# Performance work log

Measured on AMD Instinct MI355X. Metric: run time of the kernel, lower is better.

## Reference

```python
import jax, jax.numpy as jnp
import numpy as np

D_MODEL, D_INNER, D_STATE, D_CONV, DT_RANK = 192, 384, 16, 4, 12
EPS = 1e-5


def _causal_dwconv(x, w, b):
    # x: (B, L, Din); w: (Din, 1, K) depthwise; causal left pad K-1
    xc = x.transpose(0, 2, 1)  # (B, Din, L)
    y = jax.lax.conv_general_dilated(xc, w, window_strides=(1,),
                                     padding=[(D_CONV - 1, 0)],
                                     feature_group_count=D_INNER,
                                     dimension_numbers=('NCH', 'OIH', 'NCH'))
    return (y + b[None, :, None]).transpose(0, 2, 1)  # (B, L, Din)


def _ssm_dir(xh, z, conv_w, conv_b, x_proj_w, dt_w, dt_b, A_log, D):
    # one direction of the selective scan
    x = jax.nn.silu(_causal_dwconv(xh, conv_w, conv_b))  # (B, L, Din)
    x_dbl = jnp.einsum('bld,ed->ble', x, x_proj_w)       # (B, L, R+2N)
    dt = jax.nn.softplus(jnp.einsum('blr,dr->bld', x_dbl[..., :DT_RANK], dt_w) + dt_b)
    Bm = x_dbl[..., DT_RANK:DT_RANK + D_STATE]           # (B, L, N)
    Cm = x_dbl[..., DT_RANK + D_STATE:]                  # (B, L, N)
    A = -jnp.exp(A_log)                                  # (Din, N)
    deltaA = jnp.exp(dt[..., None] * A)                  # (B, L, Din, N)
    dBx = (dt * x)[..., None] * Bm[:, :, None, :]        # (B, L, Din, N)

    def comb(e1, e2):
        a1, b1 = e1
        a2, b2 = e2
        return a1 * a2, a2 * b1 + b2

    _, h = jax.lax.associative_scan(comb, (deltaA, dBx), axis=1)
    y = jnp.einsum('bldn,bln->bld', h, Cm) + x * D
    return y * jax.nn.silu(z)


def setup_inputs() -> dict:
    key = jax.random.key(0)
    ks = jax.random.split(key, 24)
    B, L = 2, 2048
    s = 0.02
    inp = {
        'hidden_states': jax.random.normal(ks[0], (B, L, D_MODEL), jnp.float32),
        'residual': jax.random.normal(ks[1], (B, L, D_MODEL), jnp.float32),
        'norm_w': jnp.ones((D_MODEL,), jnp.float32),
        'in_proj_w': jax.random.normal(ks[2], (2 * D_INNER, D_MODEL)) * s,
        'out_proj_w': jax.random.normal(ks[3], (D_MODEL, D_INNER)) * s,
        # forward-direction SSM params
        'conv_w_f': jax.random.normal(ks[4], (D_INNER, 1, D_CONV)) * s,
        'conv_b_f': jnp.zeros((D_INNER,), jnp.float32),
        'x_proj_w_f': jax.random.normal(ks[5], (DT_RANK + 2 * D_STATE, D_INNER)) * s,
        'dt_w_f': jax.random.normal(ks[6], (D_INNER, DT_RANK)) * s,
        'dt_b_f': jax.random.uniform(ks[7], (D_INNER,), minval=-4.0, maxval=-2.0),
        'A_log_f': jnp.log(jnp.tile(jnp.arange(1, D_STATE + 1, dtype=jnp.float32), (D_INNER, 1))),
        'D_f': jnp.ones((D_INNER,), jnp.float32),
        # backward-direction SSM params (bimamba)
        'conv_w_b': jax.random.normal(ks[8], (D_INNER, 1, D_CONV)) * s,
        'conv_b_b': jnp.zeros((D_INNER,), jnp.float32),
        'x_proj_w_b': jax.random.normal(ks[9], (DT_RANK + 2 * D_STATE, D_INNER)) * s,
        'dt_w_b': jax.random.normal(ks[10], (D_INNER, DT_RANK)) * s,
        'dt_b_b': jax.random.uniform(ks[11], (D_INNER,), minval=-4.0, maxval=-2.0),
        'A_log_b': jnp.log(jnp.tile(jnp.arange(1, D_STATE + 1, dtype=jnp.float32), (D_INNER, 1))),
        'D_b': jnp.ones((D_INNER,), jnp.float32),
    }
    return inp


def reference(hidden_states, residual, norm_w, in_proj_w, out_proj_w,
              conv_w_f, conv_b_f, x_proj_w_f, dt_w_f, dt_b_f, A_log_f, D_f,
              conv_w_b, conv_b_b, x_proj_w_b, dt_w_b, dt_b_b, A_log_b, D_b):
    # fused add + RMSNorm (prenorm=True): residual_out = hidden + residual (fp32)
    residual_out = (hidden_states + residual).astype(jnp.float32)
    x = residual_out * jax.lax.rsqrt(jnp.mean(residual_out * residual_out, axis=-1, keepdims=True) + EPS)
    x = x * norm_w
    # Mamba mixer, bimamba=True
    xz = jnp.einsum('bld,ed->ble', x, in_proj_w)  # (B, L, 2*Din)
    xh, z = xz[..., :D_INNER], xz[..., D_INNER:]
    y_f = _ssm_dir(xh, z, conv_w_f, conv_b_f, x_proj_w_f, dt_w_f, dt_b_f, A_log_f, D_f)
    y_b = _ssm_dir(xh[:, ::-1], z[:, ::-1], conv_w_b, conv_b_b, x_proj_w_b, dt_w_b, dt_b_b, A_log_b, D_b)[:, ::-1]
    out = jnp.einsum('bld,ed->ble', y_f + y_b, out_proj_w)
    return out, residual_out
```

## Files before the change

### kernel.cpp

```cpp
#include <hip/hip_runtime.h>
#include <math.h>

#define BB 2
#define LL 2048
#define DM 192
#define DI 384
#define DS 16
#define RK 12
#define NROW (BB*LL)
#define NCH 64
#define CLEN (LL/NCH)

typedef __attribute__((ext_vector_type(8))) short bf16x8;
typedef __attribute__((ext_vector_type(4))) float f32x4;

__device__ __forceinline__ float siluf(float v) { return v / (1.f + __expf(-v)); }

__device__ __forceinline__ unsigned short f2bf(float f) {
  unsigned int x = __float_as_uint(f);
  unsigned int r = (x + 0x7fffu + ((x >> 16) & 1u)) >> 16;
  return (unsigned short)r;
}

#define N_BFIN  (6*48*512)
#define N_BFOUT (12*12*512)
#define N_BFXP  (2*12*4*512)
#define N_DT    (2*RK*DI)
#define N_PREP  (N_BFIN + N_BFOUT + N_BFXP + N_DT)

__global__ __launch_bounds__(256) void k_wprep(
    const float* __restrict__ wip, const float* __restrict__ wop,
    const float* __restrict__ xpwf, const float* __restrict__ xpwb,
    const float* __restrict__ dtwf, const float* __restrict__ dtwb,
    unsigned short* __restrict__ bin, unsigned short* __restrict__ bout,
    unsigned short* __restrict__ bxp, float* __restrict__ wdt) {
  int i = blockIdx.x * 256 + threadIdx.x;
  if (i < N_BFIN) {
    int j = i & 7, l = (i >> 3) & 63, ng = (i >> 9) % 48, ks = i / (48 * 512);
    int k = ks * 32 + (l >> 4) * 8 + j, c = ng * 16 + (l & 15);
    bin[i] = f2bf(wip[c * DM + k]);
  } else if (i < N_BFIN + N_BFOUT) {
    int t = i - N_BFIN;
    int j = t & 7, l = (t >> 3) & 63, ng = (t >> 9) % 12, ks = t / (12 * 512);
    int k = ks * 32 + (l >> 4) * 8 + j, c = ng * 16 + (l & 15);
    bout[t] = f2bf(wop[c * DI + k]);
  } else if (i < N_BFIN + N_BFOUT + N_BFXP) {
    int t = i - N_BFIN - N_BFOUT;
    int j = t & 7, l = (t >> 3) & 63, ng = (t >> 9) & 3, ks = (t >> 11) % 12;
    int dir = t / (12 * 4 * 512);
    int k = ks * 32 + (l >> 4) * 8 + j, e = ng * 16 + (l & 15);
    const float* src = dir ? xpwb : xpwf;
    bxp[t] = (e < RK + 2 * DS) ? f2bf(src[e * DI + k]) : (unsigned short)0;
  } else if (i < N_PREP) {
    int t = i - N_BFIN - N_BFOUT - N_BFXP;
    int dir = t / (RK * DI), rem = t % (RK * DI);
    int j = rem / DI, d = rem % DI;
    const float* src = dir ? dtwb : dtwf;
    wdt[t] = src[d * RK + j];
  }
}

__global__ __launch_bounds__(256) void k_rmsnorm(
    const float* __restrict__ h, const float* __restrict__ r,
    const float* __restrict__ w, float* __restrict__ res,
    unsigned short* __restrict__ xnb) {
  int row = blockIdx.x * 4 + (threadIdx.x >> 6);
  int lane = threadIdx.x & 63;
  const float* hp = h + row * DM;
  const float* rp = r + row * DM;
  float v0 = hp[lane]       + rp[lane];
  float v1 = hp[lane + 64]  + rp[lane + 64];
  float v2 = hp[lane + 128] + rp[lane + 128];
  float ss = v0 * v0 + v1 * v1 + v2 * v2;
  #pragma unroll
  for (int o = 32; o; o >>= 1) ss += __shfl_xor(ss, o);
  float inv = rsqrtf(ss * (1.f / DM) + 1e-5f);
  float* rr = res + row * DM;
  unsigned short* xo = xnb + row * DM;
  rr[lane] = v0; rr[lane + 64] = v1; rr[lane + 128] = v2;
  xo[lane]       = f2bf(v0 * inv * w[lane]);
  xo[lane + 64]  = f2bf(v1 * inv * w[lane + 64]);
  xo[lane + 128] = f2bf(v2 * inv * w[lane + 128]);
}

__global__ __launch_bounds__(256) void k_inproj(
    const unsigned short* __restrict__ xnb, const unsigned short* __restrict__ bin,
    float* __restrict__ xh, float* __restrict__ z) {
  int l = threadIdx.x & 63, w = threadIdx.x >> 6;
  int row0 = blockIdx.x * 16;
  const unsigned short* arow = xnb + (size_t)(row0 + (l & 15)) * DM + ((l >> 4) * 8);
  f32x4 acc[12];
  #pragma unroll
  for (int g = 0; g < 12; g++) acc[g] = (f32x4){0.f, 0.f, 0.f, 0.f};
  #pragma unroll
  for (int ks = 0; ks < 6; ks++) {
    bf16x8 a = *reinterpret_cast<const bf16x8*>(arow + ks * 32);
    #pragma unroll
    for (int g = 0; g < 12; g++) {
      int ng = w * 12 + g;
      bf16x8 b = *reinterpret_cast<const bf16x8*>(bin + ((size_t)(ks * 48 + ng) * 64 + l) * 8);
      acc[g] = __builtin_amdgcn_mfma_f32_16x16x32_bf16(a, b, acc[g], 0, 0, 0);
    }
  }
  int rbase = row0 + (l >> 4) * 4;
  #pragma unroll
  for (int g = 0; g < 12; g++) {
    int col = (w * 12 + g) * 16 + (l & 15);
    float* dst = (col < DI) ? (xh + col) : (z + (col - DI));
    #pragma unroll
    for (int r = 0; r < 4; r++) dst[(size_t)(rbase + r) * DI] = acc[g][r];
  }
}

__global__ __launch_bounds__(256) void k_conv(
    const float* __restrict__ xh,
    const float* __restrict__ cwf, const float* __restrict__ cbf,
    const float* __restrict__ cwb, const float* __restrict__ cbb,
    float* __restrict__ xc, unsigned short* __restrict__ xcb) {
  int dir = blockIdx.y;
  int g = blockIdx.x * 256 + threadIdx.x;
  int row = g / DI, d = g % DI;
  int b = row >> 11, s = row & (LL - 1);
  const float* cw = dir ? cwb : cwf;
  const float* cb = dir ? cbb : cbf;
  float acc = cb[d];
  #pragma unroll
  for (int k = 0; k < 4; k++) {
    int sp = s - 3 + k;
    if (sp >= 0) {
      int mr = b * LL + (dir ? (LL - 1 - sp) : sp);
      acc += cw[d * 4 + k] * xh[(size_t)mr * DI + d];
    }
  }
  float v = siluf(acc);
  size_t idx = (size_t)(dir * NROW + row) * DI + d;
  xc[idx] = v;
  xcb[idx] = f2bf(v);
}

__global__ __launch_bounds__(64) void k_xpmm(
    const unsigned short* __restrict__ xcb, const unsigned short* __restrict__ bxp,
    float* __restrict__ xdbl) {
  int l = threadIdx.x;
  int dir = blockIdx.y;
  int row0 = blockIdx.x * 16;
  const unsigned short* arow = xcb + (size_t)(dir * NROW + row0 + (l & 15)) * DI + ((l >> 4) * 8);
  const unsigned short* wb = bxp + (size_t)dir * 12 * 4 * 512;
  f32x4 acc[4];
  #pragma unroll
  for (int g = 0; g < 4; g++) acc[g] = (f32x4){0.f, 0.f, 0.f, 0.f};
  #pragma unroll
  for (int ks = 0; ks < 12; ks++) {
    bf16x8 a = *reinterpret_cast<const bf16x8*>(arow + ks * 32);
    #pragma unroll
    for (int g = 0; g < 4; g++) {
      bf16x8 b = *reinterpret_cast<const bf16x8*>(wb + ((size_t)(ks * 4 + g) * 64 + l) * 8);
      acc[g] = __builtin_amdgcn_mfma_f32_16x16x32_bf16(a, b, acc[g], 0, 0, 0);
    }
  }
  int rbase = row0 + (l >> 4) * 4;
  #pragma unroll
  for (int g = 0; g < 4; g++) {
    int col = g * 16 + (l & 15);
    #pragma unroll
    for (int r = 0; r < 4; r++)
      xdbl[(size_t)(dir * NROW + rbase + r) * 64 + col] = acc[g][r];
  }
}

__global__ __launch_bounds__(128) void k_dtbc(
    const float* __restrict__ xdbl, const float* __restrict__ wdt_all,
    const float* __restrict__ dtbf, const float* __restrict__ dtbb,
    float* __restrict__ dt, float* __restrict__ Bm, float* __restrict__ Cm) {
  int row = blockIdx.x;
  int dir = row >> 12;
  const float* xr = xdbl + (size_t)row * 64;
  float xj[RK];
  #pragma unroll
  for (int j = 0; j < RK; j++) xj[j] = xr[j];
  const float* wdt = wdt_all + dir * RK * DI;
  const float* dtb = dir ? dtbb : dtbf;
  int t = threadIdx.x;
  #pragma unroll
  for (int it = 0; it < 3; it++) {
    int d = it * 128 + t;
    float a = dtb[d];
    #pragma unroll
    for (int j = 0; j < RK; j++) a = __fmaf_rn(xj[j], wdt[j * DI + d], a);
    a = (a > 20.f) ? a : log1pf(__expf(a));
    dt[(size_t)row * DI + d] = a;
  }
  if (t < 32) {
    float v = xr[RK + t];
    if (t < DS) Bm[(size_t)row * DS + t] = v;
    else        Cm[(size_t)row * DS + (t - DS)] = v;
  }
}

__global__ __launch_bounds__(128) void k_scan1(
    const float* __restrict__ dt, const float* __restrict__ xc,
    const float* __restrict__ Bm,
    const float* __restrict__ Alf, const float* __restrict__ Alb,
    float* __restrict__ S, float* __restrict__ P) {
  int zb = blockIdx.z;
  int dir = zb >> 1;
  int d = blockIdx.x * 128 + threadIdx.x;
  int c = blockIdx.y;
  const float* Al = dir ? Alb : Alf;
  float Av[DS];
  {
    const float4* ap = reinterpret_cast<const float4*>(Al + d * DS);
    #pragma unroll
    for (int q = 0; q < 4; q++) {
      float4 a = ap[q];
      Av[4*q+0] = -__expf(a.x); Av[4*q+1] = -__expf(a.y);
      Av[4*q+2] = -__expf(a.z); Av[4*q+3] = -__expf(a.w);
    }
  }
  int rowbase = zb * LL + c * CLEN;
  const float4* Bp4 = reinterpret_cast<const float4*>(Bm + (size_t)rowbase * DS);
  float h[DS];
  #pragma unroll
  for (int n = 0; n < DS; n++) h[n] = 0.f;
  float sdt = 0.f;
  float dtv = dt[(size_t)rowbase * DI + d];
  float xv  = xc[(size_t)rowbase * DI + d];
  #pragma unroll 4
  for (int s = 0; s < CLEN; s++) {
    float dtn_ = 0.f, xn_ = 0.f;
    if (s + 1 < CLEN) {
      dtn_ = dt[(size_t)(rowbase + s + 1) * DI + d];
      xn_  = xc[(size_t)(rowbase + s + 1) * DI + d];
    }
    float4 B0 = Bp4[s*4+0], B1 = Bp4[s*4+1], B2 = Bp4[s*4+2], B3 = Bp4[s*4+3];
    float Bv[DS] = {B0.x,B0.y,B0.z,B0.w, B1.x,B1.y,B1.z,B1.w,
                    B2.x,B2.y,B2.z,B2.w, B3.x,B3.y,B3.z,B3.w};
    float dtx = dtv * xv;
    sdt += dtv;
    #pragma unroll
    for (int n = 0; n < DS; n++) {
      float dA = __expf(dtv * Av[n]);
      h[n] = __fmaf_rn(dA, h[n], dtx * Bv[n]);
    }
    dtv = dtn_; xv = xn_;
  }
  size_t base = ((size_t)(zb * NCH + c) * DI + d) * DS;
  float4* Sp = reinterpret_cast<float4*>(S + base);
  float4* Pp = reinterpret_cast<float4*>(P + base);
  #pragma unroll
  for (int q = 0; q < 4; q++) {
    Sp[q] = make_float4(h[4*q+0], h[4*q+1], h[4*q+2], h[4*q+3]);
    Pp[q] = make_float4(__expf(Av[4*q+0]*sdt), __expf(Av[4*q+1]*sdt),
                        __expf(Av[4*q+2]*sdt), __expf(Av[4*q+3]*sdt));
  }
}

__global__ __launch_bounds__(256) void k_scan2(
    float* __restrict__ S, const float* __restrict__ P) {
  int g = blockIdx.x * 256 + threadIdx.x;
  int zb = g / (DI * DS);
  int rem = g % (DI * DS);
  const int stride = DI * DS;
  size_t base = (size_t)zb * NCH * stride + rem;
  float carry = 0.f;
  for (int c0 = 0; c0 < NCH; c0 += 8) {
    float p8[8], s8[8];
    #pragma unroll
    for (int j = 0; j < 8; j++) {
      p8[j] = P[base + (size_t)(c0 + j) * stride];
      s8[j] = S[base + (size_t)(c0 + j) * stride];
    }
    #pragma unroll
    for (int j = 0; j < 8; j++) {
      S[base + (size_t)(c0 + j) * stride] = carry;
      carry = __fmaf_rn(p8[j], carry, s8[j]);
    }
  }
}

__global__ __launch_bounds__(128) void k_scan3(
    const float* __restrict__ dt, const float* __restrict__ xc,
    const float* __restrict__ Bm, const float* __restrict__ Cm,
    const float* __restrict__ z, const float* __restrict__ Hin,
    const float* __restrict__ Alf, const float* __restrict__ Alb,
    const float* __restrict__ Df, const float* __restrict__ Db,
    float* __restrict__ y) {
  int zb = blockIdx.z;
  int dir = zb >> 1, b = zb & 1;
  int d = blockIdx.x * 128 + threadIdx.x;
  int c = blockIdx.y;
  const float* Al = dir ? Alb : Alf;
  const float* Dp = dir ? Db : Df;
  float Av[DS];
  {
    const float4* ap = reinterpret_cast<const float4*>(Al + d * DS);
    #pragma unroll
    for (int q = 0; q < 4; q++) {
      float4 a = ap[q];
      Av[4*q+0] = -__expf(a.x); Av[4*q+1] = -__expf(a.y);
      Av[4*q+2] = -__expf(a.z); Av[4*q+3] = -__expf(a.w);
    }
  }
  float Dv = Dp[d];
  int rowbase = zb * LL + c * CLEN;
  const float4* Bp4 = reinterpret_cast<const float4*>(Bm + (size_t)rowbase * DS);
  const float4* Cp4 = reinterpret_cast<const float4*>(Cm + (size_t)rowbase * DS);
  size_t base = ((size_t)(zb * NCH + c) * DI + d) * DS;
  float h[DS];
  {
    const float4* hp = reinterpret_cast<const float4*>(Hin + base);
    #pragma unroll
    for (int q = 0; q < 4; q++) {
      float4 a = hp[q];
      h[4*q+0] = a.x; h[4*q+1] = a.y; h[4*q+2] = a.z; h[4*q+3] = a.w;
    }
  }
  float dtv = dt[(size_t)rowbase * DI + d];
  float xv  = xc[(size_t)rowbase * DI + d];
  #pragma unroll 4
  for (int s = 0; s < CLEN; s++) {
    float dtn_ = 0.f, xn_ = 0.f;
    if (s + 1 < CLEN) {
      dtn_ = dt[(size_t)(rowbase + s + 1) * DI + d];
      xn_  = xc[(size_t)(rowbase + s + 1) * DI + d];
    }
    float4 B0 = Bp4[s*4+0], B1 = Bp4[s*4+1], B2 = Bp4[s*4+2], B3 = Bp4[s*4+3];
    float Bv[DS] = {B0.x,B0.y,B0.z,B0.w, B1.x,B1.y,B1.z,B1.w,
                    B2.x,B2.y,B2.z,B2.w, B3.x,B3.y,B3.z,B3.w};
    float4 C0 = Cp4[s*4+0], C1 = Cp4[s*4+1], C2 = Cp4[s*4+2], C3 = Cp4[s*4+3];
    float Cv[DS] = {C0.x,C0.y,C0.z,C0.w, C1.x,C1.y,C1.z,C1.w,
                    C2.x,C2.y,C2.z,C2.w, C3.x,C3.y,C3.z,C3.w};
    float dtx = dtv * xv;
    float acc = xv * Dv;
    #pragma unroll
    for (int n = 0; n < DS; n++) {
      float dA = __expf(dtv * Av[n]);
      h[n] = __fmaf_rn(dA, h[n], dtx * Bv[n]);
      acc = __fmaf_rn(h[n], Cv[n], acc);
    }
    int sg = c * CLEN + s;
    int mr = b * LL + (dir ? (LL - 1 - sg) : sg);
    float zv = z[(size_t)mr * DI + d];
    y[(size_t)(rowbase + s) * DI + d] = acc * siluf(zv);
    dtv = dtn_; xv = xn_;
  }
}

__global__ __launch_bounds__(128) void k_outproj(
    const float* __restrict__ y, const unsigned short* __restrict__ bout,
    float* __restrict__ out) {
  int l = threadIdx.x & 63, w = threadIdx.x >> 6;
  int row0 = blockIdx.x * 16;
  int row = row0 + (l & 15);
  int b = row >> 11, ll = row & (LL - 1);
  const float* yf = y + (size_t)(b * LL + ll) * DI + (l >> 4) * 8;
  const float* yb = y + (size_t)((2 + b) * LL + (LL - 1 - ll)) * DI + (l >> 4) * 8;
  f32x4 acc[6];
  #pragma unroll
  for (int g = 0; g < 6; g++) acc[g] = (f32x4){0.f, 0.f, 0.f, 0.f};
  #pragma unroll
  for (int ks = 0; ks < 12; ks++) {
    const float4* yf4 = reinterpret_cast<const float4*>(yf + ks * 32);
    const float4* yb4 = reinterpret_cast<const float4*>(yb + ks * 32);
    float4 f0 = yf4[0], f1 = yf4[1];
    float4 g0 = yb4[0], g1 = yb4[1];
    bf16x8 a;
    a[0] = (short)f2bf(f0.x + g0.x); a[1] = (short)f2bf(f0.y + g0.y);
    a[2] = (short)f2bf(f0.z + g0.z); a[3] = (short)f2bf(f0.w + g0.w);
    a[4] = (short)f2bf(f1.x + g1.x); a[5] = (short)f2bf(f1.y + g1.y);
    a[6] = (short)f2bf(f1.z + g1.z); a[7] = (short)f2bf(f1.w + g1.w);
    #pragma unroll
    for (int g = 0; g < 6; g++) {
      int ng = w * 6 + g;
      bf16x8 bb = *reinterpret_cast<const bf16x8*>(bout + ((size_t)(ks * 12 + ng) * 64 + l) * 8);
      acc[g] = __builtin_amdgcn_mfma_f32_16x16x32_bf16(a, bb, acc[g], 0, 0, 0);
    }
  }
  int rbase = row0 + (l >> 4) * 4;
  #pragma unroll
  for (int g = 0; g < 6; g++) {
    int col = (w * 6 + g) * 16 + (l & 15);
    #pragma unroll
    for (int r = 0; r < 4; r++) out[(size_t)(rbase + r) * DM + col] = acc[g][r];
  }
}

extern "C" void kernel_launch(void* const* d_in, const int* in_sizes, int n_in,
                              void* d_out, int out_size, void* d_ws, size_t ws_size,
                              hipStream_t stream) {
  const float* hid  = (const float*)d_in[0];
  const float* res  = (const float*)d_in[1];
  const float* nw   = (const float*)d_in[2];
  const float* wip  = (const float*)d_in[3];
  const float* wop  = (const float*)d_in[4];
  const float* cwf  = (const float*)d_in[5];
  const float* cbf  = (const float*)d_in[6];
  const float* xpwf = (const float*)d_in[7];
  const float* dtwf = (const float*)d_in[8];
  const float* dtbf = (const float*)d_in[9];
  const float* Alf  = (const float*)d_in[10];
  const float* Df   = (const float*)d_in[11];
  const float* cwb  = (const float*)d_in[12];
  const float* cbb  = (const float*)d_in[13];
  const float* xpwb = (const float*)d_in[14];
  const float* dtwb = (const float*)d_in[15];
  const float* dtbb = (const float*)d_in[16];
  const float* Alb  = (const float*)d_in[17];
  const float* Db   = (const float*)d_in[18];

  float* out_p  = (float*)d_out;
  float* resid  = out_p + NROW * DM;

  float* ws = (float*)d_ws;
  float* xh   = ws;
  float* zz   = xh   + NROW * DI;
  float* xc   = zz   + NROW * DI;
  float* dt   = xc   + 2 * NROW * DI;
  float* Bm   = dt   + 2 * NROW * DI;
  float* Cm   = Bm   + 2 * NROW * DS;
  float* yy   = Cm   + 2 * NROW * DS;
  float* S    = yy   + 2 * NROW * DI;
  float* P    = S    + 2 * BB * NCH * DI * DS;
  float* xdbl = P    + 2 * BB * NCH * DI * DS;
  float* wdt  = xdbl + 2 * NROW * 64;
  float* fend = wdt  + N_DT;
  unsigned short* xnb = (unsigned short*)fend;
  unsigned short* xcb = xnb + NROW * DM;
  unsigned short* bin = xcb + 2 * NROW * DI;
  unsigned short* bout = bin + N_BFIN;
  unsigned short* bxp  = bout + N_BFOUT;

  k_wprep<<<(N_PREP + 255) / 256, 256, 0, stream>>>(wip, wop, xpwf, xpwb, dtwf, dtwb,
                                                    bin, bout, bxp, wdt);
  k_rmsnorm<<<NROW / 4, 256, 0, stream>>>(hid, res, nw, resid, xnb);
  k_inproj<<<NROW / 16, 256, 0, stream>>>(xnb, bin, xh, zz);
  k_conv<<<dim3(NROW * DI / 256, 2), 256, 0, stream>>>(xh, cwf, cbf, cwb, cbb, xc, xcb);
  k_xpmm<<<dim3(NROW / 16, 2), 64, 0, stream>>>(xcb, bxp, xdbl);
  k_dtbc<<<2 * NROW, 128, 0, stream>>>(xdbl, wdt, dtbf, dtbb, dt, Bm, Cm);
  k_scan1<<<dim3(DI / 128, NCH, 2 * BB), 128, 0, stream>>>(dt, xc, Bm, Alf, Alb, S, P);
  k_scan2<<<(2 * BB * DI * DS) / 256, 256, 0, stream>>>(S, P);
  k_scan3<<<dim3(DI / 128, NCH, 2 * BB), 128, 0, stream>>>(dt, xc, Bm, Cm, zz, S,
                                                           Alf, Alb, Df, Db, yy);
  k_outproj<<<NROW / 16, 128, 0, stream>>>(yy, bout, out_p);
}
```

Before: 235.5 us.

## Store intermediates in bf16, fuse dt projection into x_proj GEMM, split GEMM grids

Stores the in_proj outputs (xh, z), the conv output, and the scan output y in bf16 instead of fp32. This roughly halves the memory traffic of the memory-bound conv, scan and out_proj kernels and drops the duplicate fp32 xc buffer. The dt/B/C projection kernel is fused into the x_proj MFMA kernel through shared memory, which removes the xdbl round trip and one launch. The in_proj and out_proj grids are split along output columns into smaller 64-thread blocks for more parallelism. The trade-off is lower precision in the scan inputs and in y, and in_proj now reloads the A tile once per column block.

```diff
diff --git a/kernel.cpp b/kernel.cpp
--- a/kernel.cpp
+++ b/kernel.cpp
@@ -20,6 +20,9 @@
   unsigned int x = __float_as_uint(f);
   unsigned int r = (x + 0x7fffu + ((x >> 16) & 1u)) >> 16;
   return (unsigned short)r;
+}
+__device__ __forceinline__ float bf2f(unsigned short u) {
+  return __uint_as_float(((unsigned int)u) << 16);
 }
 
 #define N_BFIN  (6*48*512)
@@ -83,40 +86,40 @@
   xo[lane + 128] = f2bf(v2 * inv * w[lane + 128]);
 }
 
-__global__ __launch_bounds__(256) void k_inproj(
+__global__ __launch_bounds__(64) void k_inproj(
     const unsigned short* __restrict__ xnb, const unsigned short* __restrict__ bin,
-    float* __restrict__ xh, float* __restrict__ z) {
-  int l = threadIdx.x & 63, w = threadIdx.x >> 6;
+    unsigned short* __restrict__ xhb, unsigned short* __restrict__ zb) {
+  int l = threadIdx.x;
   int row0 = blockIdx.x * 16;
+  int ng0 = blockIdx.y * 4;
   const unsigned short* arow = xnb + (size_t)(row0 + (l & 15)) * DM + ((l >> 4) * 8);
-  f32x4 acc[12];
-  #pragma unroll
-  for (int g = 0; g < 12; g++) acc[g] = (f32x4){0.f, 0.f, 0.f, 0.f};
+  f32x4 acc[4];
+  #pragma unroll
+  for (int g = 0; g < 4; g++) acc[g] = (f32x4){0.f, 0.f, 0.f, 0.f};
   #pragma unroll
   for (int ks = 0; ks < 6; ks++) {
     bf16x8 a = *reinterpret_cast<const bf16x8*>(arow + ks * 32);
     #pragma unroll
-    for (int g = 0; g < 12; g++) {
-      int ng = w * 12 + g;
-      bf16x8 b = *reinterpret_cast<const bf16x8*>(bin + ((size_t)(ks * 48 + ng) * 64 + l) * 8);
+    for (int g = 0; g < 4; g++) {
+      bf16x8 b = *reinterpret_cast<const bf16x8*>(bin + ((size_t)(ks * 48 + ng0 + g) * 64 + l) * 8);
       acc[g] = __builtin_amdgcn_mfma_f32_16x16x32_bf16(a, b, acc[g], 0, 0, 0);
     }
   }
   int rbase = row0 + (l >> 4) * 4;
   #pragma unroll
-  for (int g = 0; g < 12; g++) {
-    int col = (w * 12 + g) * 16 + (l & 15);
-    float* dst = (col < DI) ? (xh + col) : (z + (col - DI));
-    #pragma unroll
-    for (int r = 0; r < 4; r++) dst[(size_t)(rbase + r) * DI] = acc[g][r];
+  for (int g = 0; g < 4; g++) {
+    int col = (ng0 + g) * 16 + (l & 15);
+    unsigned short* dst = (col < DI) ? (xhb + col) : (zb + (col - DI));
+    #pragma unroll
+    for (int r = 0; r < 4; r++) dst[(size_t)(rbase + r) * DI] = f2bf(acc[g][r]);
   }
 }
 
 __global__ __launch_bounds__(256) void k_conv(
-    const float* __restrict__ xh,
+    const unsigned short* __restrict__ xhb,
     const float* __restrict__ cwf, const float* __restrict__ cbf,
     const float* __restrict__ cwb, const float* __restrict__ cbb,
-    float* __restrict__ xc, unsigned short* __restrict__ xcb) {
+    unsigned short* __restrict__ xcb) {
   int dir = blockIdx.y;
   int g = blockIdx.x * 256 + threadIdx.x;
   int row = g / DI, d = g % DI;
@@ -129,76 +132,69 @@
     int sp = s - 3 + k;
     if (sp >= 0) {
       int mr = b * LL + (dir ? (LL - 1 - sp) : sp);
-      acc += cw[d * 4 + k] * xh[(size_t)mr * DI + d];
-    }
-  }
-  float v = siluf(acc);
-  size_t idx = (size_t)(dir * NROW + row) * DI + d;
-  xc[idx] = v;
-  xcb[idx] = f2bf(v);
-}
-
-__global__ __launch_bounds__(64) void k_xpmm(
+      acc += cw[d * 4 + k] * bf2f(xhb[(size_t)mr * DI + d]);
+    }
+  }
+  xcb[(size_t)(dir * NROW + row) * DI + d] = f2bf(siluf(acc));
+}
+
+__global__ __launch_bounds__(128) void k_xpmm(
     const unsigned short* __restrict__ xcb, const unsigned short* __restrict__ bxp,
-    float* __restrict__ xdbl) {
-  int l = threadIdx.x;
+    const float* __restrict__ wdt_all,
+    const float* __restrict__ dtbf, const float* __restrict__ dtbb,
+    float* __restrict__ dt, float* __restrict__ Bm, float* __restrict__ Cm) {
+  __shared__ float xd[16][48];
+  int l = threadIdx.x & 63, w = threadIdx.x >> 6;
   int dir = blockIdx.y;
   int row0 = blockIdx.x * 16;
   const unsigned short* arow = xcb + (size_t)(dir * NROW + row0 + (l & 15)) * DI + ((l >> 4) * 8);
   const unsigned short* wb = bxp + (size_t)dir * 12 * 4 * 512;
-  f32x4 acc[4];
-  #pragma unroll
-  for (int g = 0; g < 4; g++) acc[g] = (f32x4){0.f, 0.f, 0.f, 0.f};
+  f32x4 acc[2];
+  acc[0] = (f32x4){0.f, 0.f, 0.f, 0.f};
+  acc[1] = (f32x4){0.f, 0.f, 0.f, 0.f};
   #pragma unroll
   for (int ks = 0; ks < 12; ks++) {
     bf16x8 a = *reinterpret_cast<const bf16x8*>(arow + ks * 32);
     #pragma unroll
-    for (int g = 0; g < 4; g++) {
-      bf16x8 b = *reinterpret_cast<const bf16x8*>(wb + ((size_t)(ks * 4 + g) * 64 + l) * 8);
+    for (int g = 0; g < 2; g++) {
+      int ng = w * 2 + g;
+      bf16x8 b = *reinterpret_cast<const bf16x8*>(wb + ((size_t)(ks * 4 + ng) * 64 + l) * 8);
       acc[g] = __builtin_amdgcn_mfma_f32_16x16x32_bf16(a, b, acc[g], 0, 0, 0);
     }
   }
-  int rbase = row0 + (l >> 4) * 4;
-  #pragma unroll
-  for (int g = 0; g < 4; g++) {
-    int col = g * 16 + (l & 15);
-    #pragma unroll
-    for (int r = 0; r < 4; r++)
-      xdbl[(size_t)(dir * NROW + rbase + r) * 64 + col] = acc[g][r];
-  }
-}
-
-__global__ __launch_bounds__(128) void k_dtbc(
-    const float* __restrict__ xdbl, const float* __restrict__ wdt_all,
-    const float* __restrict__ dtbf, const float* __restrict__ dtbb,
-    float* __restrict__ dt, float* __restrict__ Bm, float* __restrict__ Cm) {
-  int row = blockIdx.x;
-  int dir = row >> 12;
-  const float* xr = xdbl + (size_t)row * 64;
-  float xj[RK];
-  #pragma unroll
-  for (int j = 0; j < RK; j++) xj[j] = xr[j];
+  int rbase = (l >> 4) * 4;
+  #pragma unroll
+  for (int g = 0; g < 2; g++) {
+    int col = (w * 2 + g) * 16 + (l & 15);
+    #pragma unroll
+    for (int r = 0; r < 4; r++) xd[rbase + r][col] = acc[g][r];
+  }
+  __syncthreads();
   const float* wdt = wdt_all + dir * RK * DI;
   const float* dtb = dir ? dtbb : dtbf;
   int t = threadIdx.x;
   #pragma unroll
-  for (int it = 0; it < 3; it++) {
-    int d = it * 128 + t;
+  for (int i = 0; i < 48; i++) {
+    int idx = i * 128 + t;
+    int row = idx / DI, d = idx % DI;
     float a = dtb[d];
     #pragma unroll
-    for (int j = 0; j < RK; j++) a = __fmaf_rn(xj[j], wdt[j * DI + d], a);
+    for (int j = 0; j < RK; j++) a = __fmaf_rn(xd[row][j], wdt[j * DI + d], a);
     a = (a > 20.f) ? a : log1pf(__expf(a));
-    dt[(size_t)row * DI + d] = a;
-  }
-  if (t < 32) {
-    float v = xr[RK + t];
-    if (t < DS) Bm[(size_t)row * DS + t] = v;
-    else        Cm[(size_t)row * DS + (t - DS)] = v;
+    dt[(size_t)(dir * NROW + row0 + row) * DI + d] = a;
+  }
+  #pragma unroll
+  for (int i = 0; i < 4; i++) {
+    int idx = i * 128 + t;
+    int row = idx / 32, j = idx % 32;
+    float v = xd[row][RK + j];
+    if (j < DS) Bm[(size_t)(dir * NROW + row0 + row) * DS + j] = v;
+    else        Cm[(size_t)(dir * NROW + row0 + row) * DS + (j - DS)] = v;
   }
 }
 
 __global__ __launch_bounds__(128) void k_scan1(
-    const float* __restrict__ dt, const float* __restrict__ xc,
+    const float* __restrict__ dt, const unsigned short* __restrict__ xcb,
     const float* __restrict__ Bm,
     const float* __restrict__ Alf, const float* __restrict__ Alb,
     float* __restrict__ S, float* __restrict__ P) {
@@ -224,13 +220,13 @@
   for (int n = 0; n < DS; n++) h[n] = 0.f;
   float sdt = 0.f;
   float dtv = dt[(size_t)rowbase * DI + d];
-  float xv  = xc[(size_t)rowbase * DI + d];
+  float xv  = bf2f(xcb[(size_t)rowbase * DI + d]);
   #pragma unroll 4
   for (int s = 0; s < CLEN; s++) {
     float dtn_ = 0.f, xn_ = 0.f;
     if (s + 1 < CLEN) {
       dtn_ = dt[(size_t)(rowbase + s + 1) * DI + d];
-      xn_  = xc[(size_t)(rowbase + s + 1) * DI + d];
+      xn_  = bf2f(xcb[(size_t)(rowbase + s + 1) * DI + d]);
     }
     float4 B0 = Bp4[s*4+0], B1 = Bp4[s*4+1], B2 = Bp4[s*4+2], B3 = Bp4[s*4+3];
     float Bv[DS] = {B0.x,B0.y,B0.z,B0.w, B1.x,B1.y,B1.z,B1.w,
@@ -279,14 +275,14 @@
 }
 
 __global__ __launch_bounds__(128) void k_scan3(
-    const float* __restrict__ dt, const float* __restrict__ xc,
+    const float* __restrict__ dt, const unsigned short* __restrict__ xcb,
     const float* __restrict__ Bm, const float* __restrict__ Cm,
-    const float* __restrict__ z, const float* __restrict__ Hin,
+    const unsigned short* __restrict__ zb_, const float* __restrict__ Hin,
     const float* __restrict__ Alf, const float* __restrict__ Alb,
     const float* __restrict__ Df, const float* __restrict__ Db,
-    float* __restrict__ y) {
-  int zb = blockIdx.z;
-  int dir = zb >> 1, b = zb & 1;
+    unsigned short* __restrict__ yb) {
+  int zbi = blockIdx.z;
+  int dir = zbi >> 1, b = zbi & 1;
   int d = blockIdx.x * 128 + threadIdx.x;
   int c = blockIdx.y;
   const float* Al = dir ? Alb : Alf;
@@ -302,10 +298,10 @@
     }
   }
   float Dv = Dp[d];
-  int rowbase = zb * LL + c * CLEN;
+  int rowbase = zbi * LL + c * CLEN;
   const float4* Bp4 = reinterpret_cast<const float4*>(Bm + (size_t)rowbase * DS);
   const float4* Cp4 = reinterpret_cast<const float4*>(Cm + (size_t)rowbase * DS);
-  size_t base = ((size_t)(zb * NCH + c) * DI + d) * DS;
+  size_t base = ((size_t)(zbi * NCH + c) * DI + d) * DS;
   float h[DS];
   {
     const float4* hp = reinterpret_cast<const float4*>(Hin + base);
@@ -316,13 +312,13 @@
     }
   }
   float dtv = dt[(size_t)rowbase * DI + d];
-  float xv  = xc[(size_t)rowbase * DI + d];
+  float xv  = bf2f(xcb[(size_t)rowbase * DI + d]);
   #pragma unroll 4
   for (int s = 0; s < CLEN; s++) {
     float dtn_ = 0.f, xn_ = 0.f;
     if (s + 1 < CLEN) {
       dtn_ = dt[(size_t)(rowbase + s + 1) * DI + d];
-      xn_  = xc[(size_t)(rowbase + s + 1) * DI + d];
+      xn_  = bf2f(xcb[(size_t)(rowbase + s + 1) * DI + d]);
     }
     float4 B0 = Bp4[s*4+0], B1 = Bp4[s*4+1], B2 = Bp4[s*4+2], B3 = Bp4[s*4+3];
     float Bv[DS] = {B0.x,B0.y,B0.z,B0.w, B1.x,B1.y,B1.z,B1.w,
@@ -340,46 +336,43 @@
     }
     int sg = c * CLEN + s;
     int mr = b * LL + (dir ? (LL - 1 - sg) : sg);
-    float zv = z[(size_t)mr * DI + d];
-    y[(size_t)(rowbase + s) * DI + d] = acc * siluf(zv);
+    float zv = bf2f(zb_[(size_t)mr * DI + d]);
+    yb[(size_t)(rowbase + s) * DI + d] = f2bf(acc * siluf(zv));
     dtv = dtn_; xv = xn_;
   }
 }
 
-__global__ __launch_bounds__(128) void k_outproj(
-    const float* __restrict__ y, const unsigned short* __restrict__ bout,
+__global__ __launch_bounds__(64) void k_outproj(
+    const unsigned short* __restrict__ yb, const unsigned short* __restrict__ bout,
     float* __restrict__ out) {
-  int l = threadIdx.x & 63, w = threadIdx.x >> 6;
+  int l = threadIdx.x;
   int row0 = blockIdx.x * 16;
+  int ng0 = blockIdx.y * 2;
   int row = row0 + (l & 15);
   int b = row >> 11, ll = row & (LL - 1);
-  const float* yf = y + (size_t)(b * LL + ll) * DI + (l >> 4) * 8;
-  const float* yb = y + (size_t)((2 + b) * LL + (LL - 1 - ll)) * DI + (l >> 4) * 8;
-  f32x4 acc[6];
-  #pragma unroll
-  for (int g = 0; g < 6; g++) acc[g] = (f32x4){0.f, 0.f, 0.f, 0.f};
+  const unsigned short* yf = yb + (size_t)(b * LL + ll) * DI + (l >> 4) * 8;
+  const unsigned short* yr = yb + (size_t)((2 + b) * LL + (LL - 1 - ll)) * DI + (l >> 4) * 8;
+  f32x4 acc[2];
+  acc[0] = (f32x4){0.f, 0.f, 0.f, 0.f};
+  acc[1] = (f32x4){0.f, 0.f, 0.f, 0.f};
   #pragma unroll
   for (int ks = 0; ks < 12; ks++) {
-    const float4* yf4 = reinterpret_cast<const float4*>(yf + ks * 32);
-    const float4* yb4 = reinterpret_cast<const float4*>(yb + ks * 32);
-    float4 f0 = yf4[0], f1 = yf4[1];
-    float4 g0 = yb4[0], g1 = yb4[1];
+    bf16x8 f8 = *reinterpret_cast<const bf16x8*>(yf + ks * 32);
+    bf16x8 g8 = *reinterpret_cast<const bf16x8*>(yr + ks * 32);
     bf16x8 a;
-    a[0] = (short)f2bf(f0.x + g0.x); a[1] = (short)f2bf(f0.y + g0.y);
-    a[2] = (short)f2bf(f0.z + g0.z); a[3] = (short)f2bf(f0.w + g0.w);
-    a[4] = (short)f2bf(f1.x + g1.x); a[5] = (short)f2bf(f1.y + g1.y);
-    a[6] = (short)f2bf(f1.z + g1.z); a[7] = (short)f2bf(f1.w + g1.w);
-    #pragma unroll
-    for (int g = 0; g < 6; g++) {
-      int ng = w * 6 + g;
-      bf16x8 bb = *reinterpret_cast<const bf16x8*>(bout + ((size_t)(ks * 12 + ng) * 64 + l) * 8);
+    #pragma unroll
+    for (int j = 0; j < 8; j++)
+      a[j] = (short)f2bf(bf2f((unsigned short)f8[j]) + bf2f((unsigned short)g8[j]));
+    #pragma unroll
+    for (int g = 0; g < 2; g++) {
+      bf16x8 bb = *reinterpret_cast<const bf16x8*>(bout + ((size_t)(ks * 12 + ng0 + g) * 64 + l) * 8);
       acc[g] = __builtin_amdgcn_mfma_f32_16x16x32_bf16(a, bb, acc[g], 0, 0, 0);
     }
   }
   int rbase = row0 + (l >> 4) * 4;
   #pragma unroll
-  for (int g = 0; g < 6; g++) {
-    int col = (w * 6 + g) * 16 + (l & 15);
+  for (int g = 0; g < 2; g++) {
+    int col = (ng0 + g) * 16 + (l & 15);
     #pragma unroll
     for (int r = 0; r < 4; r++) out[(size_t)(rbase + r) * DM + col] = acc[g][r];
   }
@@ -412,34 +405,30 @@
   float* resid  = out_p + NROW * DM;
 
   float* ws = (float*)d_ws;
-  float* xh   = ws;
-  float* zz   = xh   + NROW * DI;
-  float* xc   = zz   + NROW * DI;
-  float* dt   = xc   + 2 * NROW * DI;
+  float* dt   = ws;
   float* Bm   = dt   + 2 * NROW * DI;
   float* Cm   = Bm   + 2 * NROW * DS;
-  float* yy   = Cm   + 2 * NROW * DS;
-  float* S    = yy   + 2 * NROW * DI;
+  float* S    = Cm   + 2 * NROW * DS;
   float* P    = S    + 2 * BB * NCH * DI * DS;
-  float* xdbl = P    + 2 * BB * NCH * DI * DS;
-  float* wdt  = xdbl + 2 * NROW * 64;
-  float* fend = wdt  + N_DT;
-  unsigned short* xnb = (unsigned short*)fend;
-  unsigned short* xcb = xnb + NROW * DM;
-  unsigned short* bin = xcb + 2 * NROW * DI;
+  float* wdt  = P    + 2 * BB * NCH * DI * DS;
+  unsigned short* xnb = (unsigned short*)(wdt + N_DT);
+  unsigned short* xhb = xnb + NROW * DM;
+  unsigned short* zb  = xhb + NROW * DI;
+  unsigned short* xcb = zb  + NROW * DI;
+  unsigned short* yb  = xcb + 2 * NROW * DI;
+  unsigned short* bin = yb  + 2 * NROW * DI;
   unsigned short* bout = bin + N_BFIN;
   unsigned short* bxp  = bout + N_BFOUT;
 
   k_wprep<<<(N_PREP + 255) / 256, 256, 0, stream>>>(wip, wop, xpwf, xpwb, dtwf, dtwb,
                                                     bin, bout, bxp, wdt);
   k_rmsnorm<<<NROW / 4, 256, 0, stream>>>(hid, res, nw, resid, xnb);
-  k_inproj<<<NROW / 16, 256, 0, stream>>>(xnb, bin, xh, zz);
-  k_conv<<<dim3(NROW * DI / 256, 2), 256, 0, stream>>>(xh, cwf, cbf, cwb, cbb, xc, xcb);
-  k_xpmm<<<dim3(NROW / 16, 2), 64, 0, stream>>>(xcb, bxp, xdbl);
-  k_dtbc<<<2 * NROW, 128, 0, stream>>>(xdbl, wdt, dtbf, dtbb, dt, Bm, Cm);
-  k_scan1<<<dim3(DI / 128, NCH, 2 * BB), 128, 0, stream>>>(dt, xc, Bm, Alf, Alb, S, P);
+  k_inproj<<<dim3(NROW / 16, 12), 64, 0, stream>>>(xnb, bin, xhb, zb);
+  k_conv<<<dim3(NROW * DI / 256, 2), 256, 0, stream>>>(xhb, cwf, cbf, cwb, cbb, xcb);
+  k_xpmm<<<dim3(NROW / 16, 2), 128, 0, stream>>>(xcb, bxp, wdt, dtbf, dtbb, dt, Bm, Cm);
+  k_scan1<<<dim3(DI / 128, NCH, 2 * BB), 128, 0, stream>>>(dt, xcb, Bm, Alf, Alb, S, P);
   k_scan2<<<(2 * BB * DI * DS) / 256, 256, 0, stream>>>(S, P);
-  k_scan3<<<dim3(DI / 128, NCH, 2 * BB), 128, 0, stream>>>(dt, xc, Bm, Cm, zz, S,
-                                                           Alf, Alb, Df, Db, yy);
-  k_outproj<<<NROW / 16, 128, 0, stream>>>(yy, bout, out_p);
-}
+  k_scan3<<<dim3(DI / 128, NCH, 2 * BB), 128, 0, stream>>>(dt, xcb, Bm, Cm, zb, S,
+                                                           Alf, Alb, Df, Db, yb);
+  k_outproj<<<dim3(NROW / 16, 6), 64, 0, stream>>>(yb, bout, out_p);
+}
```

After: 212.3 us. -9.8%, faster.
